# Optimization experiments

Measured on AMD Instinct MI355X. Metric: run time of the kernel, lower is better.

Reference implementation:

```python
import jax, jax.numpy as jnp
import numpy as np

B, T, C, K = 8, 4096, 256, 4  # batch, time, d_embd, k_periods


def setup_inputs() -> dict:
    key = jax.random.key(0)
    ks = jax.random.split(key, 5)
    x = jax.random.normal(ks[0], (B, T, C), jnp.float32)
    # inception stand-in: masked 3x3 conv (HWIO) + GELU
    Wc = jax.random.normal(ks[1], (3, 3, C, C), jnp.float32) * 0.02
    bc = jnp.zeros((C,), jnp.float32)
    # FeedForward params
    W1 = jax.random.normal(ks[2], (C, 4 * C), jnp.float32) * 0.02
    b1 = jnp.zeros((4 * C,), jnp.float32)
    W2 = jax.random.normal(ks[3], (4 * C, C), jnp.float32) * 0.02
    b2 = jnp.zeros((C,), jnp.float32)
    return {"x": x, "Wc": Wc, "bc": bc, "W1": W1, "b1": b1, "W2": W2, "b2": b2}


def _topk_freq_idx(x):
    # eager (concrete) period detection; shapes downstream are data-dependent,
    # exactly like the torch original (which is also not compilable as one graph)
    xf = jnp.fft.rfft(x, axis=1)[:, 1:, :]            # drop DC -> [B, T//2, C]
    amps_full = jnp.mean(jnp.abs(xf), axis=-1)        # [B, T//2]
    _, idx = jax.lax.top_k(amps_full, K)              # [B, K] indices into sliced bins
    return np.asarray(jax.device_get(idx))


def _fold(x, n):
    # vectorized per-sample 1D->2D folding with period n[b]; returns masked grid
    pad = (T - T % n) % n
    m = (T + pad) // n
    M, N = int(m.max()), int(n.max())
    nj = jnp.asarray(n)[:, None, None]                # [B,1,1]
    i = jnp.arange(M)[None, :, None]
    j = jnp.arange(N)[None, None, :]
    t = i * nj + j                                    # [B,M,N] flat time index
    valid = (j < nj) & (t < T)
    tc = jnp.clip(t, 0, T - 1)
    grid = x[jnp.arange(B)[:, None, None], tc] * valid[..., None]  # [B,M,N,C]
    mask = valid[..., None].astype(x.dtype)
    return grid, mask


def _inception(grid, mask, Wc, bc):
    y = jax.lax.conv_general_dilated(
        grid, Wc, window_strides=(1, 1), padding='SAME',
        dimension_numbers=('NHWC', 'HWIO', 'NHWC'))
    return jax.nn.gelu(y + bc, approximate=False) * mask


def _unfold(y, n):
    ts = jnp.arange(T)[None, :]
    nj = jnp.asarray(n)[:, None]
    return y[jnp.arange(B)[:, None], ts // nj, ts % nj]  # [B,T,C]


def _forward(x, Wc, bc, W1, b1, W2, b2, idx_np):
    # differentiable amplitude recomputation with fixed (closed-over) indices
    xf = jnp.fft.rfft(x, axis=1)[:, 1:, :]
    amps_full = jnp.mean(jnp.abs(xf), axis=-1)                     # [B, T//2]
    amps_k = jnp.take_along_axis(amps_full, jnp.asarray(idx_np), axis=1)  # [B,K]
    # original computes p = T // topk_index; clamp to avoid div-by-zero on idx 0
    p = np.maximum(T // np.maximum(idx_np, 1), 1)                   # [B,K] np ints
    outs = []
    for k in range(K):
        grid, mask = _fold(x, p[:, k])
        y = _inception(grid, mask, Wc, bc)
        outs.append(_unfold(y, p[:, k]))
    tf = jnp.stack(outs, axis=1)                                   # [B,K,T,C]
    h = jax.nn.gelu(tf @ W1 + b1, approximate=False) @ W2 + b2     # FeedForward
    w = jax.nn.softmax(amps_k, axis=-1)[:, :, None, None]
    return x + (h * w).sum(axis=1)


def reference(x, Wc, bc, W1, b1, W2, b2):
    idx_np = _topk_freq_idx(x)
    return _forward(x, Wc, bc, W1, b1, W2, b2, idx_np)
```

## Files before the change

### kernel.cpp

```cpp
#include <hip/hip_runtime.h>
#include <cstdint>
#include <cstddef>

#define T_LEN 4096
#define C_DIM 256
#define B_DIM 8
#define K_TOP 4

typedef __attribute__((ext_vector_type(8))) short bf16x8;
typedef __attribute__((ext_vector_type(4))) float f32x4;

__device__ __forceinline__ float gelu_fast(float x) {
    float x2 = x * x;
    float a = x * fmaf(0.071354816f, x2, 1.595769122f);
    float e = __expf(-a);
    return __fdividef(x, 1.0f + e);
}

__device__ __forceinline__ unsigned short f2bf(float f) {
    uint32_t u = __float_as_uint(f);
    uint32_t r = (u + 0x7fffu + ((u >> 16) & 1u)) >> 16;
    return (unsigned short)r;
}

__device__ __forceinline__ float bf2f(unsigned short v) {
    uint32_t u = ((uint32_t)v) << 16;
    return __uint_as_float(u);
}

typedef __attribute__((address_space(3))) uint32_t lds_u32_t;
typedef __attribute__((address_space(1))) const uint32_t gbl_u32_t;

__device__ __forceinline__ void lds_load16(const void* g, void* l) {
    __builtin_amdgcn_global_load_lds((gbl_u32_t*)g, (lds_u32_t*)l, 16, 0, 0);
}

#define BAR_VM0()                                                      \
    do {                                                               \
        asm volatile("s_waitcnt vmcnt(0) lgkmcnt(0)" ::: "memory");    \
        __builtin_amdgcn_s_barrier();                                  \
        __builtin_amdgcn_sched_barrier(0);                             \
    } while (0)
#define BAR_VM3()                                                      \
    do {                                                               \
        asm volatile("s_waitcnt vmcnt(3) lgkmcnt(0)" ::: "memory");    \
        __builtin_amdgcn_s_barrier();                                  \
        __builtin_amdgcn_sched_barrier(0);                             \
    } while (0)
#define BAR_LGKM()                                                     \
    do {                                                               \
        asm volatile("s_waitcnt lgkmcnt(0)" ::: "memory");             \
        __builtin_amdgcn_s_barrier();                                  \
        __builtin_amdgcn_sched_barrier(0);                             \
    } while (0)

#define FPAD(i) ((i) + ((i) >> 5))

__global__ __launch_bounds__(256) void cvt_x_kernel(const float4* __restrict__ x,
                                                    ushort4* __restrict__ xbf,
                                                    unsigned short* __restrict__ zbuf) {
    size_t i = (size_t)blockIdx.x * 256 + threadIdx.x;
    float4 v = x[i];
    ushort4 o;
    o.x = f2bf(v.x); o.y = f2bf(v.y); o.z = f2bf(v.z); o.w = f2bf(v.w);
    xbf[i] = o;
    if (blockIdx.x == 0 && threadIdx.x < 256) zbuf[threadIdx.x] = 0;
}

__global__ __launch_bounds__(256) void transpose_cvtx_kernel(const float* __restrict__ x,
                                                             unsigned short* __restrict__ xTb,
                                                             unsigned short* __restrict__ xbf,
                                                             unsigned short* __restrict__ zbuf) {
    __shared__ float tile[32][33];
    const int b = blockIdx.z;
    const int t0 = blockIdx.x * 32, c0 = blockIdx.y * 32;
    const int lx = threadIdx.x & 31, ly = threadIdx.x >> 5;
    const float* xp = x + (size_t)b * T_LEN * C_DIM;
    unsigned short* xbp = xbf + (size_t)b * T_LEN * C_DIM;
    unsigned short* op = xTb + (size_t)b * C_DIM * T_LEN;
    for (int rr = ly; rr < 32; rr += 8) {
        float v = xp[(size_t)(t0 + rr) * C_DIM + c0 + lx];
        tile[rr][lx] = v;
        xbp[(size_t)(t0 + rr) * C_DIM + c0 + lx] = f2bf(v);
    }
    __syncthreads();
    for (int rr = ly; rr < 32; rr += 8)
        op[(size_t)(c0 + rr) * T_LEN + t0 + lx] = f2bf(tile[lx][rr]);
    if (blockIdx.x == 0 && blockIdx.y == 0 && blockIdx.z == 0)
        zbuf[threadIdx.x] = 0;
}

__global__ __launch_bounds__(256) void repack_frag_kernel(const float* __restrict__ src,
                                                          unsigned short* __restrict__ dst,
                                                          int K, int N) {
    int idx = blockIdx.x * 256 + threadIdx.x;
    int total = (N >> 4) * (K >> 5) * 64;
    if (idx >= total) return;
    int lane = idx & 63, tile = idx >> 6;
    int ktiles = K >> 5;
    int tile_n = tile / ktiles, tile_k = tile % ktiles;
    int col = tile_n * 16 + (lane & 15);
    int k0 = tile_k * 32 + (lane >> 4) * 8;
    __align__(16) unsigned short v[8];
#pragma unroll
    for (int j = 0; j < 8; j++) v[j] = f2bf(src[(size_t)(k0 + j) * N + col]);
    *(uint4*)(dst + (size_t)idx * 8) = *(const uint4*)v;
}

__global__ __launch_bounds__(256) void transpose_cvt_kernel(const float* __restrict__ src,
                                                            unsigned short* __restrict__ dst,
                                                            int R, int C) {
    __shared__ float t[32][33];
    const int c0 = blockIdx.x * 32, r0 = blockIdx.y * 32;
    const int lx = threadIdx.x & 31, ly = threadIdx.x >> 5;
    for (int rr = ly; rr < 32; rr += 8) {
        int r = r0 + rr, c = c0 + lx;
        t[rr][lx] = (r < R && c < C) ? src[(size_t)r * C + c] : 0.0f;
    }
    __syncthreads();
    for (int rr = ly; rr < 32; rr += 8) {
        int c = c0 + rr, r = r0 + lx;
        if (r < R && c < C) dst[(size_t)c * R + r] = f2bf(t[lx][rr]);
    }
}

__global__ __launch_bounds__(256) void fft_mag_pair_kernel(const unsigned short* __restrict__ xTb,
                                                           unsigned short* __restrict__ mags) {
    const int bx = blockIdx.x;
    const int b = bx >> 7;
    const int c0 = (bx & 127) * 2;
    const int tid = threadIdx.x;

    __shared__ __align__(16) float re[4224];
    __shared__ __align__(16) float im[4224];
    __shared__ __align__(16) float twr[2048];
    __shared__ __align__(16) float twi[2048];

    for (int u = tid; u < 2048; u += 256) {
        float ang = -6.283185307179586f * (float)u / 4096.0f;
        float s, co;
        sincosf(ang, &s, &co);
        twr[u] = co;
        twi[u] = s;
    }

    {
        const uint4* r0 = (const uint4*)(xTb + ((size_t)(b * C_DIM + c0)) * T_LEN);
        const uint4* r1 = (const uint4*)(xTb + ((size_t)(b * C_DIM + c0 + 1)) * T_LEN);
        for (int e8 = tid; e8 < 512; e8 += 256) {
            uint4 v0 = r0[e8], v1 = r1[e8];
            const unsigned short* p0 = (const unsigned short*)&v0;
            const unsigned short* p1 = (const unsigned short*)&v1;
            int e = e8 * 8;
#pragma unroll
            for (int j = 0; j < 8; j++) {
                int r = (int)(__brev((unsigned)(e + j)) >> 20);
                re[FPAD(r)] = bf2f(p0[j]);
                im[FPAD(r)] = bf2f(p1[j]);
            }
        }
    }
    __syncthreads();

#pragma unroll
    for (int sp = 0; sp < 6; sp++) {
        const int h = 1 << (2 * sp);
        const int t1s = 11 - 2 * sp;
        const int t2s = 10 - 2 * sp;
        for (int j = tid; j < 1024; j += 256) {
            int p = j & (h - 1);
            int G = j >> (2 * sp);
            int base = G * 4 * h + p;
            int iA = FPAD(base), iB = FPAD(base + h);
            int iC = FPAD(base + 2 * h), iD = FPAD(base + 3 * h);
            float w1r = twr[p << t1s], w1i = twi[p << t1s];
            float w2r = twr[p << t2s], w2i = twi[p << t2s];
            float Ar = re[iA], Ai = im[iA], Br = re[iB], Bi = im[iB];
            float Cr = re[iC], Ci = im[iC], Dr = re[iD], Di = im[iD];
            float tBr = w1r * Br - w1i * Bi, tBi = w1r * Bi + w1i * Br;
            float tDr = w1r * Dr - w1i * Di, tDi = w1r * Di + w1i * Dr;
            float A1r = Ar + tBr, A1i = Ai + tBi;
            float B1r = Ar - tBr, B1i = Ai - tBi;
            float C1r = Cr + tDr, C1i = Ci + tDi;
            float D1r = Cr - tDr, D1i = Ci - tDi;
            float tCr = w2r * C1r - w2i * C1i, tCi = w2r * C1i + w2i * C1r;
            float uDr = w2r * D1r - w2i * D1i, uDi = w2r * D1i + w2i * D1r;
            float vDr = uDi, vDi = -uDr;
            re[iA] = A1r + tCr; im[iA] = A1i + tCi;
            re[iC] = A1r - tCr; im[iC] = A1i - tCi;
            re[iB] = B1r + vDr; im[iB] = B1i + vDi;
            re[iD] = B1r - vDr; im[iD] = B1i - vDi;
        }
        __syncthreads();
    }

    unsigned short* mp0 = mags + ((size_t)(b * C_DIM + c0)) * 2048;
    unsigned short* mp1 = mp0 + 2048;
    for (int u = tid; u < 2048; u += 256) {
        int f = u + 1;
        int g = 4096 - f;
        int jf = FPAD(f), jg = FPAD(g);
        float ar = re[jf], ai = im[jf];
        float br = re[jg], bi = im[jg];
        float xr = ar + br, xi = ai - bi;
        float yr = ai + bi, yi = br - ar;
        mp0[u] = f2bf(0.5f * sqrtf(xr * xr + xi * xi));
        mp1[u] = f2bf(0.5f * sqrtf(yr * yr + yi * yi));
    }
}

__global__ __launch_bounds__(256) void fft_mag_kernel(const float* __restrict__ src,
                                                      unsigned short* __restrict__ mags) {
    const int bx = blockIdx.x;
    const int b = bx >> 8;
    const int c = bx & 255;
    const int tid = threadIdx.x;

    __shared__ __align__(16) float re[4224];
    __shared__ __align__(16) float im[4224];
    __shared__ __align__(16) float twr[2048];
    __shared__ __align__(16) float twi[2048];

    for (int u = tid; u < 2048; u += 256) {
        float ang = -6.283185307179586f * (float)u / 4096.0f;
        float s, co;
        sincosf(ang, &s, &co);
        twr[u] = co;
        twi[u] = s;
    }
    for (int i = tid; i < 4224; i += 256) im[i] = 0.0f;

    const float* xp = src + (size_t)b * T_LEN * C_DIM + c;
    for (int e = tid; e < 4096; e += 256) {
        int r = (int)(__brev((unsigned)e) >> 20);
        re[FPAD(r)] = xp[(size_t)e * C_DIM];
    }
    __syncthreads();

#pragma unroll
    for (int sp = 0; sp < 6; sp++) {
        const int h = 1 << (2 * sp);
        const int t1s = 11 - 2 * sp;
        const int t2s = 10 - 2 * sp;
        for (int j = tid; j < 1024; j += 256) {
            int p = j & (h - 1);
            int G = j >> (2 * sp);
            int base = G * 4 * h + p;
            int iA = FPAD(base), iB = FPAD(base + h);
            int iC = FPAD(base + 2 * h), iD = FPAD(base + 3 * h);
            float w1r = twr[p << t1s], w1i = twi[p << t1s];
            float w2r = twr[p << t2s], w2i = twi[p << t2s];
            float Ar = re[iA], Ai = im[iA], Br = re[iB], Bi = im[iB];
            float Cr = re[iC], Ci = im[iC], Dr = re[iD], Di = im[iD];
            float tBr = w1r * Br - w1i * Bi, tBi = w1r * Bi + w1i * Br;
            float tDr = w1r * Dr - w1i * Di, tDi = w1r * Di + w1i * Dr;
            float A1r = Ar + tBr, A1i = Ai + tBi;
            float B1r = Ar - tBr, B1i = Ai - tBi;
            float C1r = Cr + tDr, C1i = Ci + tDi;
            float D1r = Cr - tDr, D1i = Ci - tDi;
            float tCr = w2r * C1r - w2i * C1i, tCi = w2r * C1i + w2i * C1r;
            float uDr = w2r * D1r - w2i * D1i, uDi = w2r * D1i + w2i * D1r;
            float vDr = uDi, vDi = -uDr;
            re[iA] = A1r + tCr; im[iA] = A1i + tCi;
            re[iC] = A1r - tCr; im[iC] = A1i - tCi;
            re[iB] = B1r + vDr; im[iB] = B1i + vDi;
            re[iD] = B1r - vDr; im[iD] = B1i - vDi;
        }
        __syncthreads();
    }

    unsigned short* mp = mags + ((size_t)(b * C_DIM + c)) * 2048;
    for (int u = tid; u < 2048; u += 256) {
        int f = FPAD(u + 1);
        mp[u] = f2bf(sqrtf(re[f] * re[f] + im[f] * im[f]));
    }
}

__global__ __launch_bounds__(256) void reduce_amps_kernel(const unsigned short* __restrict__ mags,
                                                          float* __restrict__ partial) {
    const int b = blockIdx.z, cc = blockIdx.y;
    const int u = blockIdx.x * 256 + threadIdx.x;
    const unsigned short* mp = mags + ((size_t)b * C_DIM + cc * 32) * 2048 + u;
    float s = 0.0f;
    for (int c = 0; c < 32; c++) s += bf2f(mp[(size_t)c * 2048]);
    partial[((size_t)b * 8 + cc) * 2048 + u] = s;
}

__global__ __launch_bounds__(256) void topk_kernel(const float* __restrict__ partial,
                                                   int* __restrict__ meta_p,
                                                   float* __restrict__ meta_w) {
    const int b = blockIdx.x;
    const int tid = threadIdx.x;
    __shared__ float v[2048];
    __shared__ float rv[256];
    __shared__ int ri[256];
    __shared__ float topv[K_TOP];
    __shared__ int topi[K_TOP];

    for (int u = tid; u < 2048; u += 256) {
        float s = 0.0f;
        for (int cc = 0; cc < 8; cc++) s += partial[((size_t)b * 8 + cc) * 2048 + u];
        v[u] = s * (1.0f / (float)C_DIM);
    }

    for (int k = 0; k < K_TOP; k++) {
        __syncthreads();
        float bv = -1e30f;
        int bi = 2048;
        for (int u = tid; u < 2048; u += 256) {
            float val = v[u];
            if (val > bv) { bv = val; bi = u; }
        }
        rv[tid] = bv;
        ri[tid] = bi;
        __syncthreads();
        for (int s = 128; s > 0; s >>= 1) {
            if (tid < s) {
                float ov = rv[tid + s];
                int oi = ri[tid + s];
                if (ov > rv[tid] || (ov == rv[tid] && oi < ri[tid])) {
                    rv[tid] = ov;
                    ri[tid] = oi;
                }
            }
            __syncthreads();
        }
        if (tid == 0) {
            topv[k] = rv[0];
            topi[k] = ri[0];
            v[ri[0]] = -1e30f;
        }
    }
    __syncthreads();
    if (tid == 0) {
        float mx = topv[0];
        for (int k = 1; k < K_TOP; k++) mx = fmaxf(mx, topv[k]);
        float e[K_TOP], se = 0.0f;
        for (int k = 0; k < K_TOP; k++) { e[k] = expf(topv[k] - mx); se += e[k]; }
        for (int k = 0; k < K_TOP; k++) {
            int idx = topi[k];
            int d = (idx >= 1) ? idx : 1;
            int p = T_LEN / d;
            if (p < 1) p = 1;
            meta_p[b * K_TOP + k] = p;
            meta_w[b * K_TOP + k] = e[k] / se;
        }
    }
}

__global__ __launch_bounds__(512) void conv_mfma_kernel(const unsigned short* __restrict__ xbf,
                                                        const unsigned short* __restrict__ WcT,
                                                        const float* __restrict__ bc,
                                                        const int* __restrict__ meta_p,
                                                        const unsigned short* __restrict__ zbuf,
                                                        unsigned short* __restrict__ convbufs,
                                                        size_t conv_stride, int koff) {
    const int b = blockIdx.y;
    const int kz = blockIdx.z;
    const int n = meta_p[b * K_TOP + koff + kz];
    const int row0 = blockIdx.x * 128;
    const int tid = threadIdx.x, w = tid >> 6, lane = tid & 63;
    const int wm = w >> 2, wn = w & 3;

    __shared__ __align__(16) unsigned short Al[3][128 * 32];
    __shared__ __align__(16) unsigned short Bl[3][256 * 32];

    const int ra = tid >> 2;
    const int swz = ((tid & 3) ^ ((ra >> 1) & 3)) * 8;
    int ti, tj;
    {
        int t = row0 + ra;
        ti = t / n;
        tj = t - ti * n;
    }
    const unsigned short* xb = xbf + (size_t)b * T_LEN * C_DIM;
    const unsigned short* baseB0 = WcT + (size_t)ra * 2304 + swz;
    const unsigned short* baseB1 = WcT + (size_t)(ra + 128) * 2304 + swz;

    auto computeA = [&](int q) -> const unsigned short* {
        int di = q / 3 - 1, dj = q % 3 - 1;
        int ii = ti + di, jj = tj + dj;
        int tp = ii * n + jj;
        bool ok = (jj >= 0) && (jj < n) && (ii >= 0) && (tp < T_LEN);
        return ok ? (xb + (size_t)tp * C_DIM + swz) : (zbuf + swz);
    };

    f32x4 acc[4][4];
#pragma unroll
    for (int m = 0; m < 4; m++)
#pragma unroll
        for (int nn = 0; nn < 4; nn++) acc[m][nn] = (f32x4){0.f, 0.f, 0.f, 0.f};

    const unsigned short* baseA = computeA(0);
    lds_load16(baseA, &Al[0][tid * 8]);
    lds_load16(baseB0, &Bl[0][tid * 8]);
    lds_load16(baseB1, &Bl[0][4096 + tid * 8]);
    lds_load16(baseA + 32, &Al[1][tid * 8]);
    lds_load16(baseB0 + 32, &Bl[1][tid * 8]);
    lds_load16(baseB1 + 32, &Bl[1][4096 + tid * 8]);

    int cur = 0, stb = 2;
    for (int s = 0; s < 72; s++) {
        if (s < 71) BAR_VM3();
        else        BAR_VM0();

        const int t = s + 2;
        if (t < 72) {
            if ((t & 7) == 0) baseA = computeA(t >> 3);
            lds_load16(baseA + (t & 7) * 32, &Al[stb][tid * 8]);
            lds_load16(baseB0 + (size_t)t * 32, &Bl[stb][tid * 8]);
            lds_load16(baseB1 + (size_t)t * 32, &Bl[stb][4096 + tid * 8]);
        }

        bf16x8 af[4], bfr[4];
#pragma unroll
        for (int m = 0; m < 4; m++) {
            int row = wm * 64 + m * 16 + (lane & 15);
            af[m] = *(const bf16x8*)((const char*)&Al[cur][0] + row * 64 +
                                     (((lane >> 4) * 16) ^ (((row >> 1) & 3) << 4)));
        }
#pragma unroll
        for (int nn = 0; nn < 4; nn++) {
            int rowb = wn * 64 + nn * 16 + (lane & 15);
            bfr[nn] = *(const bf16x8*)((const char*)&Bl[cur][0] + rowb * 64 +
                                       (((lane >> 4) * 16) ^ (((rowb >> 1) & 3) << 4)));
        }
        __builtin_amdgcn_s_setprio(1);
#pragma unroll
        for (int m = 0; m < 4; m++)
#pragma unroll
            for (int nn = 0; nn < 4; nn++)
                acc[m][nn] = __builtin_amdgcn_mfma_f32_16x16x32_bf16(af[m], bfr[nn], acc[m][nn], 0, 0, 0);
        __builtin_amdgcn_s_setprio(0);

        cur = (cur == 2) ? 0 : cur + 1;
        stb = (stb == 2) ? 0 : stb + 1;
    }

    unsigned short* ob = convbufs + (size_t)kz * conv_stride + (size_t)b * T_LEN * C_DIM;
#pragma unroll
    for (int nn = 0; nn < 4; nn++) {
        int col = wn * 64 + nn * 16 + (lane & 15);
        float bs = bc[col];
#pragma unroll
        for (int m = 0; m < 4; m++) {
            int rbase = row0 + wm * 64 + m * 16 + (lane >> 4) * 4;
#pragma unroll
            for (int r = 0; r < 4; r++) {
                float v = acc[m][nn][r] + bs;
                ob[(size_t)(rbase + r) * C_DIM + col] = f2bf(gelu_fast(v));
            }
        }
    }
}

template <int KCNT>
__global__ __launch_bounds__(256, 2) void fused_ff_kernel(
    const unsigned short* __restrict__ convbufs, size_t conv_stride,
    const unsigned short* __restrict__ W1frag,
    const unsigned short* __restrict__ W2frag,
    const float* __restrict__ b1,
    const float* __restrict__ b2,
    const float* __restrict__ meta_w,
    float* __restrict__ out,
    const float* __restrict__ osrc,
    float b2scale, int koff) {
    const int tid = threadIdx.x;
    const int wn = tid >> 6, lane = tid & 63;
    const int row0 = blockIdx.x * 32;
    const int b = row0 >> 12;

    __shared__ __align__(16) unsigned short Asw[KCNT * 32 * 256];
    __shared__ __align__(16) unsigned short Hsw[2][32 * 128];

    float wkv[KCNT];
#pragma unroll
    for (int kc = 0; kc < KCNT; kc++) wkv[kc] = meta_w[b * K_TOP + koff + kc];

    {
        const unsigned short* base = convbufs + (size_t)row0 * C_DIM;
#pragma unroll
        for (int u = 0; u < KCNT * 4; u++) {
            int ch = u * 256 + tid;
            int rfull = ch >> 5;
            int kc = rfull >> 5;
            int trow = rfull & 31;
            int cole = ((ch & 31) * 8) ^ ((rfull & 7) << 3);
            lds_load16(base + (size_t)kc * conv_stride + (size_t)trow * 256 + cole,
                       (unsigned short*)Asw + (size_t)ch * 8);
        }
    }

    f32x4 acc2[2][4];
#pragma unroll
    for (int t2 = 0; t2 < 2; t2++)
#pragma unroll
        for (int nn = 0; nn < 4; nn++) acc2[t2][nn] = (f32x4){0.f, 0.f, 0.f, 0.f};

    BAR_VM0();

    for (int cc = 0; cc < 8; cc++) {
        const int par = cc & 1;

        f32x4 acc1[KCNT][2][2];
#pragma unroll
        for (int kc = 0; kc < KCNT; kc++)
#pragma unroll
            for (int n2 = 0; n2 < 2; n2++)
#pragma unroll
                for (int t2 = 0; t2 < 2; t2++) acc1[kc][n2][t2] = (f32x4){0.f, 0.f, 0.f, 0.f};

        __builtin_amdgcn_s_setprio(1);
#pragma unroll
        for (int ks = 0; ks < 8; ks++) {
            bf16x8 w1f[2];
#pragma unroll
            for (int n2 = 0; n2 < 2; n2++) {
                int tile_n = cc * 8 + wn * 2 + n2;
                w1f[n2] = *(const bf16x8*)(W1frag + ((size_t)(tile_n * 8 + ks) * 64 + lane) * 8);
            }
            bf16x8 af[KCNT][2];
#pragma unroll
            for (int kc = 0; kc < KCNT; kc++)
#pragma unroll
                for (int t2 = 0; t2 < 2; t2++) {
                    int row = kc * 32 + t2 * 16 + (lane & 15);
                    af[kc][t2] = *(const bf16x8*)((const char*)Asw + row * 512 +
                                                  ((ks * 64 + (lane >> 4) * 16) ^ ((row & 7) << 4)));
                }
#pragma unroll
            for (int kc = 0; kc < KCNT; kc++)
#pragma unroll
                for (int n2 = 0; n2 < 2; n2++)
#pragma unroll
                    for (int t2 = 0; t2 < 2; t2++)
                        acc1[kc][n2][t2] = __builtin_amdgcn_mfma_f32_16x16x32_bf16(
                            w1f[n2], af[kc][t2], acc1[kc][n2][t2], 0, 0, 0);
        }
        __builtin_amdgcn_s_setprio(0);

#pragma unroll
        for (int n2 = 0; n2 < 2; n2++) {
            const int hloc = wn * 32 + n2 * 16 + (lane >> 4) * 4;
            f32x4 bb = *(const f32x4*)(b1 + cc * 128 + hloc);
#pragma unroll
            for (int t2 = 0; t2 < 2; t2++) {
                float hc[4];
#pragma unroll
                for (int r = 0; r < 4; r++) {
                    float s = 0.0f;
#pragma unroll
                    for (int kc = 0; kc < KCNT; kc++)
                        s += wkv[kc] * gelu_fast(acc1[kc][n2][t2][r] + bb[r]);
                    hc[r] = s;
                }
                uint32_t lo, hi;
                asm("v_cvt_pk_bf16_f32 %0, %1, %2" : "=v"(lo) : "v"(hc[0]), "v"(hc[1]));
                asm("v_cvt_pk_bf16_f32 %0, %1, %2" : "=v"(hi) : "v"(hc[2]), "v"(hc[3]));
                uint2 pk;
                pk.x = lo;
                pk.y = hi;
                int t = t2 * 16 + (lane & 15);
                *(uint2*)((char*)&Hsw[par][0] + t * 256 +
                          ((hloc * 2) ^ ((t & 7) << 4))) = pk;
            }
        }
        BAR_LGKM();

        __builtin_amdgcn_s_setprio(1);
#pragma unroll
        for (int ks2 = 0; ks2 < 4; ks2++) {
            bf16x8 af2[2], w2f[4];
#pragma unroll
            for (int t2 = 0; t2 < 2; t2++) {
                int row = t2 * 16 + (lane & 15);
                af2[t2] = *(const bf16x8*)((const char*)&Hsw[par][0] + row * 256 +
                                           ((ks2 * 64 + (lane >> 4) * 16) ^ ((row & 7) << 4)));
            }
#pragma unroll
            for (int nn = 0; nn < 4; nn++) {
                int tile_n = wn * 4 + nn;
                int tile_k = cc * 4 + ks2;
                w2f[nn] = *(const bf16x8*)(W2frag + ((size_t)(tile_n * 32 + tile_k) * 64 + lane) * 8);
            }
#pragma unroll
            for (int t2 = 0; t2 < 2; t2++)
#pragma unroll
                for (int nn = 0; nn < 4; nn++)
                    acc2[t2][nn] = __builtin_amdgcn_mfma_f32_16x16x32_bf16(af2[t2], w2f[nn],
                                                                           acc2[t2][nn], 0, 0, 0);
        }
        __builtin_amdgcn_s_setprio(0);
    }

#pragma unroll
    for (int nn = 0; nn < 4; nn++) {
        int col = wn * 64 + nn * 16 + (lane & 15);
        float bb = b2scale * b2[col];
#pragma unroll
        for (int t2 = 0; t2 < 2; t2++) {
            int rbase = row0 + t2 * 16 + (lane >> 4) * 4;
#pragma unroll
            for (int r = 0; r < 4; r++) {
                size_t idx = (size_t)(rbase + r) * C_DIM + col;
                out[idx] = osrc[idx] + acc2[t2][nn][r] + bb;
            }
        }
    }
}

extern "C" void kernel_launch(void* const* d_in, const int* in_sizes, int n_in,
                              void* d_out, int out_size, void* d_ws, size_t ws_size,
                              hipStream_t stream) {
    const float* x  = (const float*)d_in[0];
    const float* Wc = (const float*)d_in[1];
    const float* bc = (const float*)d_in[2];
    const float* W1 = (const float*)d_in[3];
    const float* b1 = (const float*)d_in[4];
    const float* W2 = (const float*)d_in[5];
    const float* b2 = (const float*)d_in[6];
    float* out = (float*)d_out;

    const size_t CONV_ELEMS = (size_t)B_DIM * T_LEN * C_DIM;
    const size_t CONV_BYTES = CONV_ELEMS * 2;
    const size_t MAGS_BYTES = (size_t)B_DIM * C_DIM * 2048 * 2;
    const size_t XT_BYTES = (size_t)B_DIM * T_LEN * C_DIM * 2;

    uint8_t* ws = (uint8_t*)d_ws;
    size_t off = 0;
    auto alloc = [&](size_t bytes) {
        size_t o = off;
        off = (off + bytes + 255) & ~(size_t)255;
        return o;
    };
    float* partial = (float*)(ws + alloc((size_t)B_DIM * 8 * 2048 * 4));
    int* meta_p = (int*)(ws + alloc(B_DIM * K_TOP * 4));
    float* meta_w = (float*)(ws + alloc(B_DIM * K_TOP * 4));
    unsigned short* xbf = (unsigned short*)(ws + alloc((size_t)B_DIM * T_LEN * C_DIM * 2));
    unsigned short* WcT = (unsigned short*)(ws + alloc((size_t)256 * 2304 * 2));
    unsigned short* W1frag = (unsigned short*)(ws + alloc((size_t)256 * 1024 * 2));
    unsigned short* W2frag = (unsigned short*)(ws + alloc((size_t)1024 * 256 * 2));
    unsigned short* zbuf = (unsigned short*)(ws + alloc(512));

    size_t remaining = (ws_size > off) ? (ws_size - off) : 0;
    uint8_t* regionA = ws + off;
    int tier;
    if (remaining >= 4 * CONV_BYTES) tier = 2;
    else if (remaining >= MAGS_BYTES + XT_BYTES) tier = 1;
    else tier = 0;

    unsigned short* mags = (unsigned short*)regionA;
    unsigned short* xTb = (unsigned short*)(regionA + ((tier == 2) ? CONV_BYTES : MAGS_BYTES));
    unsigned short* convbufs = (unsigned short*)regionA;
    const int use_xT = (tier >= 1);

    if (use_xT) {
        transpose_cvtx_kernel<<<dim3(T_LEN / 32, C_DIM / 32, B_DIM), 256, 0, stream>>>(
            x, xTb, xbf, zbuf);
    } else {
        cvt_x_kernel<<<dim3((B_DIM * T_LEN * C_DIM / 4) / 256), 256, 0, stream>>>(
            (const float4*)x, (ushort4*)xbf, zbuf);
    }

    transpose_cvt_kernel<<<dim3(256 / 32, 2304 / 32), 256, 0, stream>>>(Wc, WcT, 2304, 256);
    repack_frag_kernel<<<dim3(128), 256, 0, stream>>>(W1, W1frag, 256, 1024);
    repack_frag_kernel<<<dim3(128), 256, 0, stream>>>(W2, W2frag, 1024, 256);

    if (use_xT) {
        fft_mag_pair_kernel<<<dim3(B_DIM * 128), 256, 0, stream>>>(xTb, mags);
    } else {
        fft_mag_kernel<<<dim3(B_DIM * C_DIM), 256, 0, stream>>>(x, mags);
    }
    reduce_amps_kernel<<<dim3(2048 / 256, 8, B_DIM), 256, 0, stream>>>(mags, partial);
    topk_kernel<<<dim3(B_DIM), 256, 0, stream>>>(partial, meta_p, meta_w);

    if (tier == 2) {
        conv_mfma_kernel<<<dim3(32, B_DIM, K_TOP), 512, 0, stream>>>(
            xbf, WcT, bc, meta_p, zbuf, convbufs, CONV_ELEMS, 0);
        fused_ff_kernel<4><<<dim3(B_DIM * T_LEN / 32), 256, 0, stream>>>(
            convbufs, CONV_ELEMS, W1frag, W2frag, b1, b2, meta_w, out, x, 1.0f, 0);
    } else {
        for (int k = 0; k < K_TOP; k++) {
            conv_mfma_kernel<<<dim3(32, B_DIM, 1), 512, 0, stream>>>(
                xbf, WcT, bc, meta_p, zbuf, convbufs, 0, k);
            fused_ff_kernel<1><<<dim3(B_DIM * T_LEN / 32), 256, 0, stream>>>(
                convbufs, 0, W1frag, W2frag, b1, b2, meta_w, out,
                (k == 0) ? x : out, (k == K_TOP - 1) ? 1.0f : 0.0f, k);
        }
    }
}
```

Measured before the change: 367.4 us.

## Load conv weights as pre-packed MFMA fragments from global, double the row tile

The conv weight is now repacked into MFMA fragment order, and each wave reads its B fragments straight from global/L2 instead of staging them through LDS. LDS then holds only the A tile, which grows from 128 to 256 rows per block, so each thread issues two A loads per stage and keeps an 8x4 accumulator array. The grid halves to 16 row-blocks and the wait count drops to vmcnt(2). This removes LDS traffic and barriers for the weights and doubles weight reuse per block. The cost is higher register pressure, fewer blocks in flight, and exposed global-load latency on the weight fragments inside the main loop.

Result: slower. 393.3 us (+7.0%).

```diff
diff --git a/kernel.cpp b/kernel.cpp
--- a/kernel.cpp
+++ b/kernel.cpp
@@ -41,9 +41,9 @@
         __builtin_amdgcn_s_barrier();                                  \
         __builtin_amdgcn_sched_barrier(0);                             \
     } while (0)
-#define BAR_VM3()                                                      \
+#define BAR_VM2()                                                      \
     do {                                                               \
-        asm volatile("s_waitcnt vmcnt(3) lgkmcnt(0)" ::: "memory");    \
+        asm volatile("s_waitcnt vmcnt(2) lgkmcnt(0)" ::: "memory");    \
         __builtin_amdgcn_s_barrier();                                  \
         __builtin_amdgcn_sched_barrier(0);                             \
     } while (0)
@@ -105,23 +105,6 @@
 #pragma unroll
     for (int j = 0; j < 8; j++) v[j] = f2bf(src[(size_t)(k0 + j) * N + col]);
     *(uint4*)(dst + (size_t)idx * 8) = *(const uint4*)v;
-}
-
-__global__ __launch_bounds__(256) void transpose_cvt_kernel(const float* __restrict__ src,
-                                                            unsigned short* __restrict__ dst,
-                                                            int R, int C) {
-    __shared__ float t[32][33];
-    const int c0 = blockIdx.x * 32, r0 = blockIdx.y * 32;
-    const int lx = threadIdx.x & 31, ly = threadIdx.x >> 5;
-    for (int rr = ly; rr < 32; rr += 8) {
-        int r = r0 + rr, c = c0 + lx;
-        t[rr][lx] = (r < R && c < C) ? src[(size_t)r * C + c] : 0.0f;
-    }
-    __syncthreads();
-    for (int rr = ly; rr < 32; rr += 8) {
-        int c = c0 + rr, r = r0 + lx;
-        if (r < R && c < C) dst[(size_t)c * R + r] = f2bf(t[lx][rr]);
-    }
 }
 
 __global__ __launch_bounds__(256) void fft_mag_pair_kernel(const unsigned short* __restrict__ xTb,
@@ -349,7 +332,7 @@
 }
 
 __global__ __launch_bounds__(512) void conv_mfma_kernel(const unsigned short* __restrict__ xbf,
-                                                        const unsigned short* __restrict__ WcT,
+                                                        const unsigned short* __restrict__ WcFrag,
                                                         const float* __restrict__ bc,
                                                         const int* __restrict__ meta_p,
                                                         const unsigned short* __restrict__ zbuf,
@@ -358,79 +341,83 @@
     const int b = blockIdx.y;
     const int kz = blockIdx.z;
     const int n = meta_p[b * K_TOP + koff + kz];
-    const int row0 = blockIdx.x * 128;
+    const int row0 = blockIdx.x * 256;
     const int tid = threadIdx.x, w = tid >> 6, lane = tid & 63;
     const int wm = w >> 2, wn = w & 3;
 
-    __shared__ __align__(16) unsigned short Al[3][128 * 32];
-    __shared__ __align__(16) unsigned short Bl[3][256 * 32];
+    __shared__ __align__(16) unsigned short Al[3][256 * 32];
 
     const int ra = tid >> 2;
     const int swz = ((tid & 3) ^ ((ra >> 1) & 3)) * 8;
-    int ti, tj;
-    {
-        int t = row0 + ra;
-        ti = t / n;
-        tj = t - ti * n;
+    int ti[2], tj[2];
+#pragma unroll
+    for (int s01 = 0; s01 < 2; s01++) {
+        int t = row0 + ra + s01 * 128;
+        ti[s01] = t / n;
+        tj[s01] = t - ti[s01] * n;
     }
     const unsigned short* xb = xbf + (size_t)b * T_LEN * C_DIM;
-    const unsigned short* baseB0 = WcT + (size_t)ra * 2304 + swz;
-    const unsigned short* baseB1 = WcT + (size_t)(ra + 128) * 2304 + swz;
-
-    auto computeA = [&](int q) -> const unsigned short* {
+    const unsigned short* baseA0;
+    const unsigned short* baseA1;
+
+    auto computeA = [&](int q, int s01) -> const unsigned short* {
         int di = q / 3 - 1, dj = q % 3 - 1;
-        int ii = ti + di, jj = tj + dj;
+        int ii = ti[s01] + di, jj = tj[s01] + dj;
         int tp = ii * n + jj;
         bool ok = (jj >= 0) && (jj < n) && (ii >= 0) && (tp < T_LEN);
         return ok ? (xb + (size_t)tp * C_DIM + swz) : (zbuf + swz);
     };
 
-    f32x4 acc[4][4];
-#pragma unroll
-    for (int m = 0; m < 4; m++)
+    const unsigned short* Wb[4];
+#pragma unroll
+    for (int nn = 0; nn < 4; nn++)
+        Wb[nn] = WcFrag + (((size_t)(wn * 4 + nn) * 72) * 64 + lane) * 8;
+
+    f32x4 acc[8][4];
+#pragma unroll
+    for (int m = 0; m < 8; m++)
 #pragma unroll
         for (int nn = 0; nn < 4; nn++) acc[m][nn] = (f32x4){0.f, 0.f, 0.f, 0.f};
 
-    const unsigned short* baseA = computeA(0);
-    lds_load16(baseA, &Al[0][tid * 8]);
-    lds_load16(baseB0, &Bl[0][tid * 8]);
-    lds_load16(baseB1, &Bl[0][4096 + tid * 8]);
-    lds_load16(baseA + 32, &Al[1][tid * 8]);
-    lds_load16(baseB0 + 32, &Bl[1][tid * 8]);
-    lds_load16(baseB1 + 32, &Bl[1][4096 + tid * 8]);
+    baseA0 = computeA(0, 0);
+    baseA1 = computeA(0, 1);
+#pragma unroll
+    for (int t = 0; t < 2; t++) {
+        lds_load16(baseA0 + t * 32, &Al[t][tid * 8]);
+        lds_load16(baseA1 + t * 32, &Al[t][(tid + 512) * 8]);
+    }
 
     int cur = 0, stb = 2;
     for (int s = 0; s < 72; s++) {
-        if (s < 71) BAR_VM3();
-        else        BAR_VM0();
+        BAR_VM2();
+
+        bf16x8 bfr[4];
+#pragma unroll
+        for (int nn = 0; nn < 4; nn++)
+            bfr[nn] = *(const bf16x8*)(Wb[nn] + (size_t)s * 512);
 
         const int t = s + 2;
         if (t < 72) {
-            if ((t & 7) == 0) baseA = computeA(t >> 3);
-            lds_load16(baseA + (t & 7) * 32, &Al[stb][tid * 8]);
-            lds_load16(baseB0 + (size_t)t * 32, &Bl[stb][tid * 8]);
-            lds_load16(baseB1 + (size_t)t * 32, &Bl[stb][4096 + tid * 8]);
-        }
-
-        bf16x8 af[4], bfr[4];
-#pragma unroll
-        for (int m = 0; m < 4; m++) {
-            int row = wm * 64 + m * 16 + (lane & 15);
-            af[m] = *(const bf16x8*)((const char*)&Al[cur][0] + row * 64 +
-                                     (((lane >> 4) * 16) ^ (((row >> 1) & 3) << 4)));
-        }
-#pragma unroll
-        for (int nn = 0; nn < 4; nn++) {
-            int rowb = wn * 64 + nn * 16 + (lane & 15);
-            bfr[nn] = *(const bf16x8*)((const char*)&Bl[cur][0] + rowb * 64 +
-                                       (((lane >> 4) * 16) ^ (((rowb >> 1) & 3) << 4)));
-        }
+            if ((t & 7) == 0) {
+                int q = t >> 3;
+                baseA0 = computeA(q, 0);
+                baseA1 = computeA(q, 1);
+            }
+            const int ko = (t & 7) * 32;
+            lds_load16(baseA0 + ko, &Al[stb][tid * 8]);
+            lds_load16(baseA1 + ko, &Al[stb][(tid + 512) * 8]);
+        }
+
         __builtin_amdgcn_s_setprio(1);
 #pragma unroll
-        for (int m = 0; m < 4; m++)
+        for (int m = 0; m < 8; m++) {
+            int row = wm * 128 + m * 16 + (lane & 15);
+            bf16x8 af = *(const bf16x8*)((const char*)&Al[cur][0] + row * 64 +
+                                         (((lane >> 4) * 16) ^ (((row >> 1) & 3) << 4)));
 #pragma unroll
             for (int nn = 0; nn < 4; nn++)
-                acc[m][nn] = __builtin_amdgcn_mfma_f32_16x16x32_bf16(af[m], bfr[nn], acc[m][nn], 0, 0, 0);
+                acc[m][nn] = __builtin_amdgcn_mfma_f32_16x16x32_bf16(af, bfr[nn], acc[m][nn], 0, 0, 0);
+        }
         __builtin_amdgcn_s_setprio(0);
 
         cur = (cur == 2) ? 0 : cur + 1;
@@ -443,8 +430,8 @@
         int col = wn * 64 + nn * 16 + (lane & 15);
         float bs = bc[col];
 #pragma unroll
-        for (int m = 0; m < 4; m++) {
-            int rbase = row0 + wm * 64 + m * 16 + (lane >> 4) * 4;
+        for (int m = 0; m < 8; m++) {
+            int rbase = row0 + wm * 128 + m * 16 + (lane >> 4) * 4;
 #pragma unroll
             for (int r = 0; r < 4; r++) {
                 float v = acc[m][nn][r] + bs;
@@ -637,7 +624,7 @@
     int* meta_p = (int*)(ws + alloc(B_DIM * K_TOP * 4));
     float* meta_w = (float*)(ws + alloc(B_DIM * K_TOP * 4));
     unsigned short* xbf = (unsigned short*)(ws + alloc((size_t)B_DIM * T_LEN * C_DIM * 2));
-    unsigned short* WcT = (unsigned short*)(ws + alloc((size_t)256 * 2304 * 2));
+    unsigned short* WcFrag = (unsigned short*)(ws + alloc((size_t)2304 * 256 * 2));
     unsigned short* W1frag = (unsigned short*)(ws + alloc((size_t)256 * 1024 * 2));
     unsigned short* W2frag = (unsigned short*)(ws + alloc((size_t)1024 * 256 * 2));
     unsigned short* zbuf = (unsigned short*)(ws + alloc(512));
@@ -662,7 +649,7 @@
             (const float4*)x, (ushort4*)xbf, zbuf);
     }
 
-    transpose_cvt_kernel<<<dim3(256 / 32, 2304 / 32), 256, 0, stream>>>(Wc, WcT, 2304, 256);
+    repack_frag_kernel<<<dim3(288), 256, 0, stream>>>(Wc, WcFrag, 2304, 256);
     repack_frag_kernel<<<dim3(128), 256, 0, stream>>>(W1, W1frag, 256, 1024);
     repack_frag_kernel<<<dim3(128), 256, 0, stream>>>(W2, W2frag, 1024, 256);
 
@@ -675,14 +662,14 @@
     topk_kernel<<<dim3(B_DIM), 256, 0, stream>>>(partial, meta_p, meta_w);
 
     if (tier == 2) {
-        conv_mfma_kernel<<<dim3(32, B_DIM, K_TOP), 512, 0, stream>>>(
-            xbf, WcT, bc, meta_p, zbuf, convbufs, CONV_ELEMS, 0);
+        conv_mfma_kernel<<<dim3(16, B_DIM, K_TOP), 512, 0, stream>>>(
+            xbf, WcFrag, bc, meta_p, zbuf, convbufs, CONV_ELEMS, 0);
         fused_ff_kernel<4><<<dim3(B_DIM * T_LEN / 32), 256, 0, stream>>>(
             convbufs, CONV_ELEMS, W1frag, W2frag, b1, b2, meta_w, out, x, 1.0f, 0);
     } else {
         for (int k = 0; k < K_TOP; k++) {
-            conv_mfma_kernel<<<dim3(32, B_DIM, 1), 512, 0, stream>>>(
-                xbf, WcT, bc, meta_p, zbuf, convbufs, 0, k);
+            conv_mfma_kernel<<<dim3(16, B_DIM, 1), 512, 0, stream>>>(
+                xbf, WcFrag, bc, meta_p, zbuf, convbufs, 0, k);
             fused_ff_kernel<1><<<dim3(B_DIM * T_LEN / 32), 256, 0, stream>>>(
                 convbufs, 0, W1frag, W2frag, b1, b2, meta_w, out,
                 (k == 0) ? x : out, (k == K_TOP - 1) ? 1.0f : 0.0f, k);
```
